# Performance work log

Hardware: AMD Instinct MI355X
Metric: run time of the kernel (lower is better)

The kernel has to match this reference:

```python
import jax, jax.numpy as jnp
import numpy as np

N = 100000      # nodes
NE = 1250000    # edges
D = 64          # in_dim == out_dim
H = 8           # heads
DH = D // H     # per-head dim


def setup_inputs() -> dict:
    key = jax.random.key(0)
    ks = jax.random.split(key, 7)
    s = 1.0 / np.sqrt(D)
    return {
        "x": jax.random.normal(ks[0], (N, D), jnp.float32),
        "edge_attr": jax.random.normal(ks[1], (NE, D), jnp.float32),
        "WQ": jax.random.normal(ks[2], (D, D), jnp.float32) * s,
        "WK": jax.random.normal(ks[3], (D, D), jnp.float32) * s,
        "WV": jax.random.normal(ks[4], (D, D), jnp.float32) * s,
        "WE": jax.random.normal(ks[5], (D, D), jnp.float32) * s,
        "edge_index": jax.random.randint(ks[6], (2, NE), 0, N, dtype=jnp.int32),
    }


def reference(x, edge_attr, WQ, WK, WV, WE, edge_index):
    # Linear projections (torch Linear y = x W^T; here W is stored [in,out])
    Q = (x @ WQ).reshape(N, H, DH)
    K = (x @ WK).reshape(N, H, DH)
    V = (x @ WV).reshape(N, H, DH)
    Ef = (edge_attr @ WE).reshape(NE, H, DH)

    src = edge_index[0]
    dst = edge_index[1]

    # per-edge score: exp(clamp(sum_d K[src]*Q[dst]*E / sqrt(DH), -5, 5))
    score = (K[src] * Q[dst]) * (1.0 / np.sqrt(DH)) * Ef  # [E,H,DH]
    score = jnp.exp(jnp.clip(score.sum(-1, keepdims=True), -5.0, 5.0))  # [E,H,1]

    msg = V[src] * score  # [E,H,DH]
    wV = jax.ops.segment_sum(msg, dst, num_segments=N)    # [N,H,DH]
    Z = jax.ops.segment_sum(score, dst, num_segments=N)   # [N,H,1]

    h_out = wV / (Z + 1e-6)
    return h_out.reshape(N, H * DH)
```

## Files before the change

### kernel.cpp

```cpp
#include <hip/hip_runtime.h>
#include <hip/hip_bf16.h>

#define NN    100000
#define NEDGE 1250000

typedef __attribute__((ext_vector_type(8))) short bf16x8;
typedef __attribute__((ext_vector_type(8))) unsigned short u16x8;
typedef __attribute__((ext_vector_type(4))) float f32x4;

__device__ __forceinline__ short f2bf(float f) {
    unsigned u = __float_as_uint(f);
    u += 0x7FFFu + ((u >> 16) & 1u);
    return (short)(u >> 16);
}
__device__ __forceinline__ float bf2f(unsigned short u) {
    return __uint_as_float(((unsigned)u) << 16);
}

constexpr size_t OFF_QB   = 0;
constexpr size_t OFF_KB   = OFF_QB   + (size_t)NN * 64 * 2;
constexpr size_t OFF_VB   = OFF_KB   + (size_t)NN * 64 * 2;
constexpr size_t OFF_SRT  = OFF_VB   + (size_t)NN * 64 * 2;
constexpr size_t OFF_HIST = OFF_SRT  + (size_t)NEDGE * 8;
constexpr size_t OFF_EX   = OFF_HIST + (size_t)NN * 4;
constexpr size_t OFF_BSUM = OFF_EX   + (size_t)NN * 4;
constexpr size_t OFF_START= OFF_BSUM + 512 * 4;
constexpr size_t OFF_CUR  = OFF_START+ (size_t)(NN + 1) * 4;
constexpr size_t WS_NEED  = OFF_CUR  + (size_t)NN * 4;
constexpr int NB_SCAN = (NN + 255) / 256;

__global__ __launch_bounds__(256) void qkv_kernel(
    const float* __restrict__ x,
    const float* __restrict__ WQ, const float* __restrict__ WK,
    const float* __restrict__ WV,
    unsigned short* __restrict__ Qb, unsigned short* __restrict__ Kb,
    unsigned short* __restrict__ Vb, int* __restrict__ hist)
{
    if (hist) {
        for (int i = blockIdx.x * blockDim.x + threadIdx.x; i < NN;
             i += gridDim.x * blockDim.x)
            hist[i] = 0;
    }

    const int lane = threadIdx.x & 63;
    const int wid  = threadIdx.x >> 6;
    const int gw   = blockIdx.x * 4 + wid;
    const int nw   = gridDim.x * 4;
    const int colb = lane & 15;
    const int krow = (lane >> 4) * 8;

    bf16x8 Bf[3][4][2];
    const float* Ws[3] = {WQ, WK, WV};
    #pragma unroll
    for (int m = 0; m < 3; ++m)
        #pragma unroll
        for (int n = 0; n < 4; ++n)
            #pragma unroll
            for (int kh = 0; kh < 2; ++kh) {
                bf16x8 b;
                #pragma unroll
                for (int j = 0; j < 8; ++j)
                    b[j] = f2bf(Ws[m][(size_t)(kh * 32 + krow + j) * 64 + n * 16 + colb]);
                Bf[m][n][kh] = b;
            }

    unsigned short* Outs[3] = {Qb, Kb, Vb};

    for (int tile = gw; tile < NN / 16; tile += nw) {
        const int r0 = tile * 16;
        const float* xr = x + (size_t)(r0 + colb) * 64 + krow;
        f32x4 a0 = *(const f32x4*)(xr);
        f32x4 a1 = *(const f32x4*)(xr + 4);
        f32x4 a2 = *(const f32x4*)(xr + 32);
        f32x4 a3 = *(const f32x4*)(xr + 36);
        bf16x8 Alo, Ahi;
        #pragma unroll
        for (int j = 0; j < 4; ++j) {
            Alo[j]     = f2bf(a0[j]);
            Alo[4 + j] = f2bf(a1[j]);
            Ahi[j]     = f2bf(a2[j]);
            Ahi[4 + j] = f2bf(a3[j]);
        }
        #pragma unroll
        for (int m = 0; m < 3; ++m) {
            #pragma unroll
            for (int n = 0; n < 4; ++n) {
                f32x4 acc = {0.f, 0.f, 0.f, 0.f};
                acc = __builtin_amdgcn_mfma_f32_16x16x32_bf16(Alo, Bf[m][n][0], acc, 0, 0, 0);
                acc = __builtin_amdgcn_mfma_f32_16x16x32_bf16(Ahi, Bf[m][n][1], acc, 0, 0, 0);
                #pragma unroll
                for (int q = 0; q < 4; ++q)
                    Outs[m][(size_t)(r0 + (lane >> 4) * 4 + q) * 64 + n * 16 + colb] =
                        (unsigned short)f2bf(acc[q]);
            }
        }
    }
}

__global__ void hist_kernel(const int* __restrict__ ei, int* __restrict__ hist) {
    const int e = blockIdx.x * blockDim.x + threadIdx.x;
    if (e < NEDGE) atomicAdd(&hist[ei[NEDGE + e]], 1);
}

__global__ __launch_bounds__(256) void scanA_kernel(
    const int* __restrict__ hist, int* __restrict__ ex, int* __restrict__ bsum)
{
    __shared__ int wsum[4];
    const int i = blockIdx.x * 256 + threadIdx.x;
    const int lane = threadIdx.x & 63, wid = threadIdx.x >> 6;
    const int v = (i < NN) ? hist[i] : 0;
    int incl = v;
    #pragma unroll
    for (int off = 1; off < 64; off <<= 1) {
        int t = __shfl_up(incl, off);
        if (lane >= off) incl += t;
    }
    if (lane == 63) wsum[wid] = incl;
    __syncthreads();
    int pre = 0, bt = 0;
    #pragma unroll
    for (int w = 0; w < 4; ++w) { int s = wsum[w]; bt += s; if (w < wid) pre += s; }
    if (i < NN) ex[i] = incl - v + pre;
    if (threadIdx.x == 0) bsum[blockIdx.x] = bt;
}

__global__ __launch_bounds__(256) void scanC_kernel(
    const int* __restrict__ ex, const int* __restrict__ bsum,
    int* __restrict__ start, int* __restrict__ cursor)
{
    __shared__ int sboff;
    const int b   = blockIdx.x;
    const int tid = threadIdx.x;
    if (tid < 64) {
        int p = 0;
        for (int j = tid; j < b; j += 64) p += bsum[j];
        #pragma unroll
        for (int off = 32; off >= 1; off >>= 1) p += __shfl_down(p, off);
        if (tid == 0) sboff = p;
    }
    __syncthreads();
    const int i = b * 256 + tid;
    if (i < NN) {
        const int s = ex[i] + sboff;
        start[i] = s;
        cursor[i] = s;
    } else if (i == NN) {
        start[NN] = NEDGE;
    }
}

__global__ void scatter_kernel(const int* __restrict__ ei, int* __restrict__ cursor,
                               int2* __restrict__ sorted)
{
    const int e = blockIdx.x * blockDim.x + threadIdx.x;
    if (e < NEDGE) {
        const int dst = ei[NEDGE + e];
        const int pos = atomicAdd(&cursor[dst], 1);
        sorted[pos] = make_int2(ei[e], e);
    }
}

__global__ __launch_bounds__(256) void agg_kernel(
    const unsigned short* __restrict__ Qb, const unsigned short* __restrict__ Kb,
    const unsigned short* __restrict__ Vb,
    const float* __restrict__ edge_attr, const float* __restrict__ WE,
    const int* __restrict__ start, const int2* __restrict__ sorted,
    float* __restrict__ out)
{
    const int lane = threadIdx.x & 63;
    const int wid  = threadIdx.x >> 6;
    const int gw   = (blockIdx.x * blockDim.x + threadIdx.x) >> 6;
    const int nw   = (gridDim.x * blockDim.x) >> 6;
    const int colb = lane & 15;
    const int krow = (lane >> 4) * 8;
    const int el   = lane >> 3;
    const int h    = lane & 7;
    const float c  = 0.35355339059327373f;

    __shared__ float efs_all[4][16][68];
    float (*efs)[68] = efs_all[wid];

    bf16x8 Bf[4][2];
    #pragma unroll
    for (int n = 0; n < 4; ++n)
        #pragma unroll
        for (int kh = 0; kh < 2; ++kh) {
            bf16x8 b;
            #pragma unroll
            for (int j = 0; j < 8; ++j)
                b[j] = f2bf(WE[(size_t)(kh * 32 + krow + j) * 64 + n * 16 + colb]);
            Bf[n][kh] = b;
        }

    int dst = gw;
    int beg = 0, end = 0;
    int2 se = make_int2(0, 0);
    f32x4 a0 = {0,0,0,0}, a1 = {0,0,0,0}, a2 = {0,0,0,0}, a3 = {0,0,0,0};
    if (dst < NN) {
        beg = start[dst]; end = start[dst + 1];
        int rpos = beg + colb;
        if (rpos >= end) rpos = beg;
        if (rpos >= NEDGE) rpos = 0;
        se = sorted[rpos];
        const float* ear = edge_attr + (size_t)se.y * 64 + krow;
        a0 = *(const f32x4*)(ear);
        a1 = *(const f32x4*)(ear + 4);
        a2 = *(const f32x4*)(ear + 32);
        a3 = *(const f32x4*)(ear + 36);
    }

    for (; dst < NN; dst += nw) {
        const int dn = dst + nw;
        int beg_n = 0, end_n = 0;
        if (dn < NN) { beg_n = start[dn]; end_n = start[dn + 1]; }

        const int s0 = __shfl(se.x, el);
        const int s1 = __shfl(se.x, el + 8);
        const u16x8 k0v = *(const u16x8*)(Kb + (size_t)s0 * 64 + h * 8);
        const u16x8 v0v = *(const u16x8*)(Vb + (size_t)s0 * 64 + h * 8);
        const u16x8 k1v = *(const u16x8*)(Kb + (size_t)s1 * 64 + h * 8);
        const u16x8 v1v = *(const u16x8*)(Vb + (size_t)s1 * 64 + h * 8);
        const u16x8 qv  = *(const u16x8*)(Qb + (size_t)dst * 64 + h * 8);

        bf16x8 Alo, Ahi;
        #pragma unroll
        for (int jj = 0; jj < 4; ++jj) {
            Alo[jj]     = f2bf(a0[jj]);
            Alo[4 + jj] = f2bf(a1[jj]);
            Ahi[jj]     = f2bf(a2[jj]);
            Ahi[4 + jj] = f2bf(a3[jj]);
        }
        const int rbase = (lane >> 4) * 4;
        #pragma unroll
        for (int n = 0; n < 4; ++n) {
            f32x4 z = {0.f, 0.f, 0.f, 0.f};
            z = __builtin_amdgcn_mfma_f32_16x16x32_bf16(Alo, Bf[n][0], z, 0, 0, 0);
            z = __builtin_amdgcn_mfma_f32_16x16x32_bf16(Ahi, Bf[n][1], z, 0, 0, 0);
            #pragma unroll
            for (int q = 0; q < 4; ++q)
                efs[rbase + q][n * 16 + colb] = z[q];
        }

        int2 se_n = make_int2(0, 0);
        f32x4 a0n = {0,0,0,0}, a1n = {0,0,0,0}, a2n = {0,0,0,0}, a3n = {0,0,0,0};
        if (dn < NN) {
            int rpos_n = beg_n + colb;
            if (rpos_n >= end_n) rpos_n = beg_n;
            if (rpos_n >= NEDGE) rpos_n = 0;
            se_n = sorted[rpos_n];
            const float* earn = edge_attr + (size_t)se_n.y * 64 + krow;
            a0n = *(const f32x4*)(earn);
            a1n = *(const f32x4*)(earn + 4);
            a2n = *(const f32x4*)(earn + 32);
            a3n = *(const f32x4*)(earn + 36);
        }

        asm volatile("s_waitcnt lgkmcnt(0)" ::: "memory");
        __builtin_amdgcn_sched_barrier(0);

        f32x4 q0, q1;
        #pragma unroll
        for (int d = 0; d < 4; ++d) { q0[d] = bf2f(qv[d]); q1[d] = bf2f(qv[4 + d]); }

        f32x4 av0 = {0,0,0,0}, av1 = {0,0,0,0};
        float az = 0.f;
        {
            const f32x4 e00 = *(const f32x4*)(&efs[el][h * 8]);
            const f32x4 e01 = *(const f32x4*)(&efs[el][h * 8 + 4]);
            const f32x4 e10 = *(const f32x4*)(&efs[el + 8][h * 8]);
            const f32x4 e11 = *(const f32x4*)(&efs[el + 8][h * 8 + 4]);
            float t0 = 0.f, t1 = 0.f;
            #pragma unroll
            for (int d = 0; d < 4; ++d) {
                t0 += bf2f(k0v[d])     * q0[d] * e00[d];
                t0 += bf2f(k0v[4 + d]) * q1[d] * e01[d];
                t1 += bf2f(k1v[d])     * q0[d] * e10[d];
                t1 += bf2f(k1v[4 + d]) * q1[d] * e11[d];
            }
            const bool act0 = (beg + el)     < end;
            const bool act1 = (beg + el + 8) < end;
            const float sc0 = act0 ? __expf(fminf(fmaxf(t0 * c, -5.f), 5.f)) : 0.f;
            const float sc1 = act1 ? __expf(fminf(fmaxf(t1 * c, -5.f), 5.f)) : 0.f;
            az += sc0 + sc1;
            #pragma unroll
            for (int d = 0; d < 4; ++d) {
                av0[d] += bf2f(v0v[d])     * sc0 + bf2f(v1v[d])     * sc1;
                av1[d] += bf2f(v0v[4 + d]) * sc0 + bf2f(v1v[4 + d]) * sc1;
            }
        }

        for (int j = beg + 16; j < end; j += 16) {
            int rpos = j + colb;
            if (rpos >= end) rpos = beg;
            const int2 seb = sorted[rpos];
            const int sb0 = __shfl(seb.x, el);
            const int sb1 = __shfl(seb.x, el + 8);
            const u16x8 kb0 = *(const u16x8*)(Kb + (size_t)sb0 * 64 + h * 8);
            const u16x8 vb0 = *(const u16x8*)(Vb + (size_t)sb0 * 64 + h * 8);
            const u16x8 kb1 = *(const u16x8*)(Kb + (size_t)sb1 * 64 + h * 8);
            const u16x8 vb1 = *(const u16x8*)(Vb + (size_t)sb1 * 64 + h * 8);
            const float* earb = edge_attr + (size_t)seb.y * 64 + krow;
            const f32x4 c0 = *(const f32x4*)(earb);
            const f32x4 c1 = *(const f32x4*)(earb + 4);
            const f32x4 c2 = *(const f32x4*)(earb + 32);
            const f32x4 c3 = *(const f32x4*)(earb + 36);
            bf16x8 Blo, Bhi;
            #pragma unroll
            for (int jj = 0; jj < 4; ++jj) {
                Blo[jj]     = f2bf(c0[jj]);
                Blo[4 + jj] = f2bf(c1[jj]);
                Bhi[jj]     = f2bf(c2[jj]);
                Bhi[4 + jj] = f2bf(c3[jj]);
            }
            #pragma unroll
            for (int n = 0; n < 4; ++n) {
                f32x4 z = {0.f, 0.f, 0.f, 0.f};
                z = __builtin_amdgcn_mfma_f32_16x16x32_bf16(Blo, Bf[n][0], z, 0, 0, 0);
                z = __builtin_amdgcn_mfma_f32_16x16x32_bf16(Bhi, Bf[n][1], z, 0, 0, 0);
                #pragma unroll
                for (int q = 0; q < 4; ++q)
                    efs[rbase + q][n * 16 + colb] = z[q];
            }
            asm volatile("s_waitcnt lgkmcnt(0)" ::: "memory");
            __builtin_amdgcn_sched_barrier(0);
            const f32x4 e00 = *(const f32x4*)(&efs[el][h * 8]);
            const f32x4 e01 = *(const f32x4*)(&efs[el][h * 8 + 4]);
            const f32x4 e10 = *(const f32x4*)(&efs[el + 8][h * 8]);
            const f32x4 e11 = *(const f32x4*)(&efs[el + 8][h * 8 + 4]);
            float t0 = 0.f, t1 = 0.f;
            #pragma unroll
            for (int d = 0; d < 4; ++d) {
                t0 += bf2f(kb0[d])     * q0[d] * e00[d];
                t0 += bf2f(kb0[4 + d]) * q1[d] * e01[d];
                t1 += bf2f(kb1[d])     * q0[d] * e10[d];
                t1 += bf2f(kb1[4 + d]) * q1[d] * e11[d];
            }
            const bool act0 = (j + el)     < end;
            const bool act1 = (j + el + 8) < end;
            const float sc0 = act0 ? __expf(fminf(fmaxf(t0 * c, -5.f), 5.f)) : 0.f;
            const float sc1 = act1 ? __expf(fminf(fmaxf(t1 * c, -5.f), 5.f)) : 0.f;
            az += sc0 + sc1;
            #pragma unroll
            for (int d = 0; d < 4; ++d) {
                av0[d] += bf2f(vb0[d])     * sc0 + bf2f(vb1[d])     * sc1;
                av1[d] += bf2f(vb0[4 + d]) * sc0 + bf2f(vb1[4 + d]) * sc1;
            }
        }

        #pragma unroll
        for (int off = 8; off < 64; off <<= 1) {
            az += __shfl_xor(az, off);
            #pragma unroll
            for (int d = 0; d < 4; ++d) {
                av0[d] += __shfl_xor(av0[d], off);
                av1[d] += __shfl_xor(av1[d], off);
            }
        }

        if (el == 0) {
            const float inv = 1.f / (az + 1e-6f);
            f32x4 o0, o1;
            #pragma unroll
            for (int d = 0; d < 4; ++d) { o0[d] = av0[d] * inv; o1[d] = av1[d] * inv; }
            float* op = out + (size_t)dst * 64 + h * 8;
            *(f32x4*)(op)     = o0;
            *(f32x4*)(op + 4) = o1;
        }

        beg = beg_n; end = end_n; se = se_n;
        a0 = a0n; a1 = a1n; a2 = a2n; a3 = a3n;
    }
}

__global__ __launch_bounds__(256) void edge_kernel_fb(
    const float* __restrict__ edge_attr, const float* __restrict__ WE,
    const unsigned short* __restrict__ Qb, const unsigned short* __restrict__ Kb,
    const unsigned short* __restrict__ Vb, const int* __restrict__ ei,
    float* __restrict__ outAcc, float* __restrict__ Z)
{
    const int lane = threadIdx.x & 63;
    const int wid  = threadIdx.x >> 6;
    const int gw   = blockIdx.x * 4 + wid;
    const int nw   = gridDim.x * 4;
    const int colb = lane & 15;
    const int krow = (lane >> 4) * 8;
    const int b8   = (lane >> 3) & 1;

    bf16x8 Bf[4][2];
    #pragma unroll
    for (int n = 0; n < 4; ++n)
        #pragma unroll
        for (int kh = 0; kh < 2; ++kh) {
            bf16x8 b;
            #pragma unroll
            for (int j = 0; j < 8; ++j)
                b[j] = f2bf(WE[(size_t)(kh * 32 + krow + j) * 64 + n * 16 + colb]);
            Bf[n][kh] = b;
        }

    const float inv_sqrt_dh = 0.35355339059327373f;

    for (int tile = gw; tile < NEDGE / 16; tile += nw) {
        const int e0 = tile * 16;
        const float* ear = edge_attr + (size_t)(e0 + colb) * 64 + krow;
        f32x4 a0 = *(const f32x4*)(ear);
        f32x4 a1 = *(const f32x4*)(ear + 4);
        f32x4 a2 = *(const f32x4*)(ear + 32);
        f32x4 a3 = *(const f32x4*)(ear + 36);
        bf16x8 Alo, Ahi;
        #pragma unroll
        for (int j = 0; j < 4; ++j) {
            Alo[j]     = f2bf(a0[j]);
            Alo[4 + j] = f2bf(a1[j]);
            Ahi[j]     = f2bf(a2[j]);
            Ahi[4 + j] = f2bf(a3[j]);
        }
        f32x4 acc[4];
        #pragma unroll
        for (int n = 0; n < 4; ++n) {
            f32x4 z = {0.f, 0.f, 0.f, 0.f};
            z = __builtin_amdgcn_mfma_f32_16x16x32_bf16(Alo, Bf[n][0], z, 0, 0, 0);
            z = __builtin_amdgcn_mfma_f32_16x16x32_bf16(Ahi, Bf[n][1], z, 0, 0, 0);
            acc[n] = z;
        }
        int srcq[4], dstq[4];
        #pragma unroll
        for (int q = 0; q < 4; ++q) {
            const int erl = (lane >> 4) * 4 + q;
            srcq[q] = ei[e0 + erl];
            dstq[q] = ei[NEDGE + e0 + erl];
        }
        float sc[4][4];
        #pragma unroll
        for (int q = 0; q < 4; ++q) {
            #pragma unroll
            for (int n = 0; n < 4; ++n) {
                const int cidx = n * 16 + colb;
                const float kv = bf2f(Kb[(size_t)srcq[q] * 64 + cidx]);
                const float qv = bf2f(Qb[(size_t)dstq[q] * 64 + cidx]);
                float t = kv * qv * acc[n][q];
                t += __shfl_xor(t, 1);
                t += __shfl_xor(t, 2);
                t += __shfl_xor(t, 4);
                const float s = fminf(fmaxf(t * inv_sqrt_dh, -5.0f), 5.0f);
                sc[q][n] = __expf(s);
            }
        }
        #pragma unroll
        for (int q = 0; q < 4; ++q) {
            #pragma unroll
            for (int n = 0; n < 4; ++n) {
                const int cidx = n * 16 + colb;
                const float vv = bf2f(Vb[(size_t)srcq[q] * 64 + cidx]);
                unsafeAtomicAdd(&outAcc[(size_t)dstq[q] * 64 + cidx], vv * sc[q][n]);
                if ((lane & 7) == 0) {
                    const int hh = 2 * n + b8;
                    unsafeAtomicAdd(&Z[(size_t)dstq[q] * 8 + hh], sc[q][n]);
                }
            }
        }
    }
}

__global__ void finalize_fb(float* __restrict__ out, const float* __restrict__ Z) {
    const int i = blockIdx.x * blockDim.x + threadIdx.x;
    if (i < NN * 64) {
        const int node = i >> 6;
        const int h    = (i >> 3) & 7;
        out[i] = out[i] / (Z[node * 8 + h] + 1e-6f);
    }
}

extern "C" void kernel_launch(void* const* d_in, const int* in_sizes, int n_in,
                              void* d_out, int out_size, void* d_ws, size_t ws_size,
                              hipStream_t stream) {
    const float* x         = (const float*)d_in[0];
    const float* edge_attr = (const float*)d_in[1];
    const float* WQ        = (const float*)d_in[2];
    const float* WK        = (const float*)d_in[3];
    const float* WV        = (const float*)d_in[4];
    const float* WE        = (const float*)d_in[5];
    const int*   ei        = (const int*)d_in[6];
    float* out = (float*)d_out;

    char* base = (char*)d_ws;
    unsigned short* Qb = (unsigned short*)(base + OFF_QB);
    unsigned short* Kb = (unsigned short*)(base + OFF_KB);
    unsigned short* Vb = (unsigned short*)(base + OFF_VB);

    if (ws_size >= WS_NEED) {
        int2* sorted = (int2*)(base + OFF_SRT);
        int* hist    = (int*)(base + OFF_HIST);
        int* ex      = (int*)(base + OFF_EX);
        int* bsum    = (int*)(base + OFF_BSUM);
        int* start   = (int*)(base + OFF_START);
        int* cursor  = (int*)(base + OFF_CUR);

        qkv_kernel<<<1563, 256, 0, stream>>>(x, WQ, WK, WV, Qb, Kb, Vb, hist);
        hist_kernel<<<(NEDGE + 255) / 256, 256, 0, stream>>>(ei, hist);
        scanA_kernel<<<NB_SCAN, 256, 0, stream>>>(hist, ex, bsum);
        scanC_kernel<<<NB_SCAN, 256, 0, stream>>>(ex, bsum, start, cursor);
        scatter_kernel<<<(NEDGE + 255) / 256, 256, 0, stream>>>(ei, cursor, sorted);
        agg_kernel<<<4096, 256, 0, stream>>>(Qb, Kb, Vb, edge_attr, WE, start, sorted, out);
    } else {
        float* Z = (float*)(base + OFF_SRT);
        qkv_kernel<<<1563, 256, 0, stream>>>(x, WQ, WK, WV, Qb, Kb, Vb, nullptr);
        hipMemsetAsync(d_out, 0, (size_t)NN * 64 * sizeof(float), stream);
        hipMemsetAsync(Z, 0, (size_t)NN * 8 * sizeof(float), stream);
        edge_kernel_fb<<<2048, 256, 0, stream>>>(edge_attr, WE, Qb, Kb, Vb, ei, out, Z);
        finalize_fb<<<(NN * 64 + 255) / 256, 256, 0, stream>>>(out, Z);
    }
}
```

Measured before the change: 315.5 us.

## Permute edge_attr into dst-sorted bf16 buffer during scatter

The scatter kernel now converts each edge's fp32 attributes to bf16 and writes them at the edge's sorted position, along with a src-only index array. The aggregation kernel then reads contiguous bf16 edge features instead of gathering fp32 rows through an edge id. This replaces random fp32 gathers with coalesced half-size reads in the aggregation stage. The cost is an extra full pass over edge_attr in scatter that writes a larger workspace, and the workspace requirement grows, which may push execution onto the fallback path.

```diff
diff --git a/kernel.cpp b/kernel.cpp
--- a/kernel.cpp
+++ b/kernel.cpp
@@ -20,8 +20,9 @@
 constexpr size_t OFF_QB   = 0;
 constexpr size_t OFF_KB   = OFF_QB   + (size_t)NN * 64 * 2;
 constexpr size_t OFF_VB   = OFF_KB   + (size_t)NN * 64 * 2;
-constexpr size_t OFF_SRT  = OFF_VB   + (size_t)NN * 64 * 2;
-constexpr size_t OFF_HIST = OFF_SRT  + (size_t)NEDGE * 8;
+constexpr size_t OFF_EAS  = OFF_VB   + (size_t)NN * 64 * 2;
+constexpr size_t OFF_SSRC = OFF_EAS  + (size_t)NEDGE * 64 * 2;
+constexpr size_t OFF_HIST = OFF_SSRC + (size_t)NEDGE * 4;
 constexpr size_t OFF_EX   = OFF_HIST + (size_t)NN * 4;
 constexpr size_t OFF_BSUM = OFF_EX   + (size_t)NN * 4;
 constexpr size_t OFF_START= OFF_BSUM + 512 * 4;
@@ -149,22 +150,52 @@
     }
 }
 
-__global__ void scatter_kernel(const int* __restrict__ ei, int* __restrict__ cursor,
-                               int2* __restrict__ sorted)
+__global__ __launch_bounds__(256) void scatter_permute_kernel(
+    const int* __restrict__ ei, const float* __restrict__ edge_attr,
+    int* __restrict__ cursor, int* __restrict__ ssrc,
+    unsigned short* __restrict__ eas)
 {
-    const int e = blockIdx.x * blockDim.x + threadIdx.x;
-    if (e < NEDGE) {
-        const int dst = ei[NEDGE + e];
-        const int pos = atomicAdd(&cursor[dst], 1);
-        sorted[pos] = make_int2(ei[e], e);
+    const int lane = threadIdx.x & 63;
+    const int gw   = (blockIdx.x * blockDim.x + threadIdx.x) >> 6;
+    const int nwv  = (gridDim.x * blockDim.x) >> 6;
+    const int colb = lane & 15;
+    const int kq   = lane >> 4;
+
+    for (int tile = gw; tile < NEDGE / 16; tile += nwv) {
+        const int e0 = tile * 16;
+        const int e  = e0 + colb;
+        int pos = 0;
+        if (lane < 16) {
+            const int dst = ei[NEDGE + e];
+            pos = atomicAdd(&cursor[dst], 1);
+            ssrc[pos] = ei[e];
+        }
+        const int posb = __shfl(pos, colb);
+
+        const float* src = edge_attr + (size_t)e * 64 + kq * 16;
+        const f32x4 r0 = *(const f32x4*)(src);
+        const f32x4 r1 = *(const f32x4*)(src + 4);
+        const f32x4 r2 = *(const f32x4*)(src + 8);
+        const f32x4 r3 = *(const f32x4*)(src + 12);
+        u16x8 w0, w1;
+        #pragma unroll
+        for (int d = 0; d < 4; ++d) {
+            w0[d]     = (unsigned short)f2bf(r0[d]);
+            w0[4 + d] = (unsigned short)f2bf(r1[d]);
+            w1[d]     = (unsigned short)f2bf(r2[d]);
+            w1[4 + d] = (unsigned short)f2bf(r3[d]);
+        }
+        unsigned short* dp = eas + (size_t)posb * 64 + kq * 16;
+        *(u16x8*)(dp)     = w0;
+        *(u16x8*)(dp + 8) = w1;
     }
 }
 
 __global__ __launch_bounds__(256) void agg_kernel(
     const unsigned short* __restrict__ Qb, const unsigned short* __restrict__ Kb,
     const unsigned short* __restrict__ Vb,
-    const float* __restrict__ edge_attr, const float* __restrict__ WE,
-    const int* __restrict__ start, const int2* __restrict__ sorted,
+    const unsigned short* __restrict__ eas, const float* __restrict__ WE,
+    const int* __restrict__ start, const int* __restrict__ ssrc,
     float* __restrict__ out)
 {
     const int lane = threadIdx.x & 63;
@@ -193,20 +224,16 @@
         }
 
     int dst = gw;
-    int beg = 0, end = 0;
-    int2 se = make_int2(0, 0);
-    f32x4 a0 = {0,0,0,0}, a1 = {0,0,0,0}, a2 = {0,0,0,0}, a3 = {0,0,0,0};
-    if (dst < NN) {
-        beg = start[dst]; end = start[dst + 1];
+    int beg = start[dst], end = start[dst + 1];
+    int srcv;
+    bf16x8 Alo, Ahi;
+    {
         int rpos = beg + colb;
         if (rpos >= end) rpos = beg;
         if (rpos >= NEDGE) rpos = 0;
-        se = sorted[rpos];
-        const float* ear = edge_attr + (size_t)se.y * 64 + krow;
-        a0 = *(const f32x4*)(ear);
-        a1 = *(const f32x4*)(ear + 4);
-        a2 = *(const f32x4*)(ear + 32);
-        a3 = *(const f32x4*)(ear + 36);
+        srcv = ssrc[rpos];
+        Alo = *(const bf16x8*)(eas + (size_t)rpos * 64 + krow);
+        Ahi = *(const bf16x8*)(eas + (size_t)rpos * 64 + 32 + krow);
     }
 
     for (; dst < NN; dst += nw) {
@@ -214,22 +241,14 @@
         int beg_n = 0, end_n = 0;
         if (dn < NN) { beg_n = start[dn]; end_n = start[dn + 1]; }
 
-        const int s0 = __shfl(se.x, el);
-        const int s1 = __shfl(se.x, el + 8);
+        const int s0 = __shfl(srcv, el);
+        const int s1 = __shfl(srcv, el + 8);
         const u16x8 k0v = *(const u16x8*)(Kb + (size_t)s0 * 64 + h * 8);
         const u16x8 v0v = *(const u16x8*)(Vb + (size_t)s0 * 64 + h * 8);
         const u16x8 k1v = *(const u16x8*)(Kb + (size_t)s1 * 64 + h * 8);
         const u16x8 v1v = *(const u16x8*)(Vb + (size_t)s1 * 64 + h * 8);
         const u16x8 qv  = *(const u16x8*)(Qb + (size_t)dst * 64 + h * 8);
 
-        bf16x8 Alo, Ahi;
-        #pragma unroll
-        for (int jj = 0; jj < 4; ++jj) {
-            Alo[jj]     = f2bf(a0[jj]);
-            Alo[4 + jj] = f2bf(a1[jj]);
-            Ahi[jj]     = f2bf(a2[jj]);
-            Ahi[4 + jj] = f2bf(a3[jj]);
-        }
         const int rbase = (lane >> 4) * 4;
         #pragma unroll
         for (int n = 0; n < 4; ++n) {
@@ -241,18 +260,15 @@
                 efs[rbase + q][n * 16 + colb] = z[q];
         }
 
-        int2 se_n = make_int2(0, 0);
-        f32x4 a0n = {0,0,0,0}, a1n = {0,0,0,0}, a2n = {0,0,0,0}, a3n = {0,0,0,0};
+        int srcv_n = 0;
+        bf16x8 Alon = {}, Ahin = {};
         if (dn < NN) {
             int rpos_n = beg_n + colb;
             if (rpos_n >= end_n) rpos_n = beg_n;
             if (rpos_n >= NEDGE) rpos_n = 0;
-            se_n = sorted[rpos_n];
-            const float* earn = edge_attr + (size_t)se_n.y * 64 + krow;
-            a0n = *(const f32x4*)(earn);
-            a1n = *(const f32x4*)(earn + 4);
-            a2n = *(const f32x4*)(earn + 32);
-            a3n = *(const f32x4*)(earn + 36);
+            srcv_n = ssrc[rpos_n];
+            Alon = *(const bf16x8*)(eas + (size_t)rpos_n * 64 + krow);
+            Ahin = *(const bf16x8*)(eas + (size_t)rpos_n * 64 + 32 + krow);
         }
 
         asm volatile("s_waitcnt lgkmcnt(0)" ::: "memory");
@@ -292,26 +308,15 @@
         for (int j = beg + 16; j < end; j += 16) {
             int rpos = j + colb;
             if (rpos >= end) rpos = beg;
-            const int2 seb = sorted[rpos];
-            const int sb0 = __shfl(seb.x, el);
-            const int sb1 = __shfl(seb.x, el + 8);
+            const int sv = ssrc[rpos];
+            const bf16x8 Blo = *(const bf16x8*)(eas + (size_t)rpos * 64 + krow);
+            const bf16x8 Bhi = *(const bf16x8*)(eas + (size_t)rpos * 64 + 32 + krow);
+            const int sb0 = __shfl(sv, el);
+            const int sb1 = __shfl(sv, el + 8);
             const u16x8 kb0 = *(const u16x8*)(Kb + (size_t)sb0 * 64 + h * 8);
             const u16x8 vb0 = *(const u16x8*)(Vb + (size_t)sb0 * 64 + h * 8);
             const u16x8 kb1 = *(const u16x8*)(Kb + (size_t)sb1 * 64 + h * 8);
             const u16x8 vb1 = *(const u16x8*)(Vb + (size_t)sb1 * 64 + h * 8);
-            const float* earb = edge_attr + (size_t)seb.y * 64 + krow;
-            const f32x4 c0 = *(const f32x4*)(earb);
-            const f32x4 c1 = *(const f32x4*)(earb + 4);
-            const f32x4 c2 = *(const f32x4*)(earb + 32);
-            const f32x4 c3 = *(const f32x4*)(earb + 36);
-            bf16x8 Blo, Bhi;
-            #pragma unroll
-            for (int jj = 0; jj < 4; ++jj) {
-                Blo[jj]     = f2bf(c0[jj]);
-                Blo[4 + jj] = f2bf(c1[jj]);
-                Bhi[jj]     = f2bf(c2[jj]);
-                Bhi[4 + jj] = f2bf(c3[jj]);
-            }
             #pragma unroll
             for (int n = 0; n < 4; ++n) {
                 f32x4 z = {0.f, 0.f, 0.f, 0.f};
@@ -367,8 +372,8 @@
             *(f32x4*)(op + 4) = o1;
         }
 
-        beg = beg_n; end = end_n; se = se_n;
-        a0 = a0n; a1 = a1n; a2 = a2n; a3 = a3n;
+        beg = beg_n; end = end_n; srcv = srcv_n;
+        Alo = Alon; Ahi = Ahin;
     }
 }
 
@@ -489,21 +494,22 @@
     unsigned short* Vb = (unsigned short*)(base + OFF_VB);
 
     if (ws_size >= WS_NEED) {
-        int2* sorted = (int2*)(base + OFF_SRT);
-        int* hist    = (int*)(base + OFF_HIST);
-        int* ex      = (int*)(base + OFF_EX);
-        int* bsum    = (int*)(base + OFF_BSUM);
-        int* start   = (int*)(base + OFF_START);
-        int* cursor  = (int*)(base + OFF_CUR);
+        unsigned short* eas = (unsigned short*)(base + OFF_EAS);
+        int* ssrc   = (int*)(base + OFF_SSRC);
+        int* hist   = (int*)(base + OFF_HIST);
+        int* ex     = (int*)(base + OFF_EX);
+        int* bsum   = (int*)(base + OFF_BSUM);
+        int* start  = (int*)(base + OFF_START);
+        int* cursor = (int*)(base + OFF_CUR);
 
         qkv_kernel<<<1563, 256, 0, stream>>>(x, WQ, WK, WV, Qb, Kb, Vb, hist);
         hist_kernel<<<(NEDGE + 255) / 256, 256, 0, stream>>>(ei, hist);
         scanA_kernel<<<NB_SCAN, 256, 0, stream>>>(hist, ex, bsum);
         scanC_kernel<<<NB_SCAN, 256, 0, stream>>>(ex, bsum, start, cursor);
-        scatter_kernel<<<(NEDGE + 255) / 256, 256, 0, stream>>>(ei, cursor, sorted);
-        agg_kernel<<<4096, 256, 0, stream>>>(Qb, Kb, Vb, edge_attr, WE, start, sorted, out);
+        scatter_permute_kernel<<<4096, 256, 0, stream>>>(ei, edge_attr, cursor, ssrc, eas);
+        agg_kernel<<<4096, 256, 0, stream>>>(Qb, Kb, Vb, eas, WE, start, ssrc, out);
     } else {
-        float* Z = (float*)(base + OFF_SRT);
+        float* Z = (float*)(base + OFF_EAS);
         qkv_kernel<<<1563, 256, 0, stream>>>(x, WQ, WK, WV, Qb, Kb, Vb, nullptr);
         hipMemsetAsync(d_out, 0, (size_t)NN * 64 * sizeof(float), stream);
         hipMemsetAsync(Z, 0, (size_t)NN * 8 * sizeof(float), stream);
```

New measurement: 315.9 us. No clear change (+0.1%).
